# Performance work log

Hardware: AMD Instinct MI355X
Metric: run time of the kernel (lower is better)

The kernel has to match this reference:

```python
import jax, jax.numpy as jnp
import numpy as np

HID, H, D, DFF = 128, 4, 128, 2048   # hidden_dim, nheads, out_feats per head, dim_feedforward
N, E, B = 32768, 524288, 32
EPS = 1e-5
SLOPE = 0.2  # DGL EdgeGATConv negative_slope default


def setup_inputs() -> dict:
    key = jax.random.key(0)
    ks = jax.random.split(key, 16)
    s = 0.05
    return {
        "h": jax.random.normal(ks[0], (N, HID), jnp.float32),
        "e": jax.random.normal(ks[1], (E, 1), jnp.float32),
        "src": jax.random.randint(ks[2], (E,), 0, N, jnp.int32),
        "dst": jax.random.randint(ks[3], (E,), 0, N, jnp.int32),
        "batch_size": B,
        # EdgeGATConv params (fc / fc_edge / res_fc are bias-free in DGL)
        "W_fc": jax.random.normal(ks[4], (HID, H * D), jnp.float32) * s,
        "attn_l": jax.random.normal(ks[5], (H, D), jnp.float32) * s,
        "attn_r": jax.random.normal(ks[6], (H, D), jnp.float32) * s,
        "W_fe": jax.random.normal(ks[7], (1, H * D), jnp.float32) * s,
        "attn_e": jax.random.normal(ks[8], (H, D), jnp.float32) * s,
        "W_res": jax.random.normal(ks[9], (HID, H * D), jnp.float32) * s,
        "gat_bias": jnp.zeros((H * D,), jnp.float32),
        # linear_mha + norms + FFN
        "W_mha": jax.random.normal(ks[10], (H * D, HID), jnp.float32) * s,
        "b_mha": jnp.zeros((HID,), jnp.float32),
        "n1_g": jnp.ones((HID,), jnp.float32),
        "n1_b": jnp.zeros((HID,), jnp.float32),
        "n2_g": jnp.ones((HID,), jnp.float32),
        "n2_b": jnp.zeros((HID,), jnp.float32),
        "W1": jax.random.normal(ks[11], (HID, DFF), jnp.float32) * s,
        "b1": jnp.zeros((DFF,), jnp.float32),
        "W2": jax.random.normal(ks[12], (DFF, HID), jnp.float32) * s,
        "b2": jnp.zeros((HID,), jnp.float32),
    }


def _ln(x, g, b):
    mu = x.mean(-1, keepdims=True)
    var = ((x - mu) ** 2).mean(-1, keepdims=True)
    return (x - mu) * jax.lax.rsqrt(var + EPS) * g + b


def reference(h, e, src, dst, batch_size, W_fc, attn_l, attn_r, W_fe, attn_e,
              W_res, gat_bias, W_mha, b_mha, n1_g, n1_b, n2_g, n2_b,
              W1, b1, W2, b2):
    n = h.shape[0]
    h0 = h
    # --- EdgeGATConv (eval mode: dropouts are identity) ---
    ft = (h @ W_fc).reshape(n, H, D)                         # (N,H,D)
    el = jnp.einsum("nhd,hd->nh", ft, attn_l)                # (N,H)
    er = jnp.einsum("nhd,hd->nh", ft, attn_r)
    fe = (e @ W_fe).reshape(-1, H, D)                        # (E,H,D)
    ee = jnp.einsum("ehd,hd->eh", fe, attn_e)                # (E,H)
    sc = jax.nn.leaky_relu(el[src] + er[dst] + ee, SLOPE)    # (E,H)
    # segment softmax over incoming edges of each dst node
    m = jax.ops.segment_max(sc, dst, num_segments=n)         # (N,H)
    m = jnp.where(jnp.isfinite(m), m, 0.0)                   # empty segments
    w = jnp.exp(sc - m[dst])
    z = jax.ops.segment_sum(w, dst, num_segments=n)
    zd = z[dst]
    alpha = w / jnp.where(zd == 0, 1.0, zd)                  # (E,H)
    msg = ft[src] * alpha[:, :, None]                        # (E,H,D)
    rst = jax.ops.segment_sum(msg, dst, num_segments=n)      # (N,H,D)
    rst = rst + (h0 @ W_res).reshape(n, H, D) + gat_bias.reshape(1, H, D)
    # --- transformer wrapper ---
    x = jax.nn.relu(rst).reshape(n, H * D)
    x = jax.nn.relu(x @ W_mha + b_mha)
    x = _ln(h0 + x, n1_g, n1_b)
    x = x.reshape(batch_size, -1, x.shape[1])                # (B, N/B, HID)
    ff = jax.nn.relu(x @ W1 + b1) @ W2 + b2
    return _ln(x + ff, n2_g, n2_b)
```

## Files before the change

kernel.cpp:

```cpp
#include <hip/hip_runtime.h>
#include <hip/hip_bf16.h>

#define N_NODES 32768
#define E_EDGES 524288
#define HIDDIM 128
#define FDIM 512
#define DFF 2048
#define LN_EPS 1e-5f
#define SLOPE 0.2f
#define CAP 64

typedef __bf16 bf16_t;
typedef __bf16 bf16x8 __attribute__((ext_vector_type(8)));
typedef float f32x4 __attribute__((ext_vector_type(4)));
typedef float f32x2 __attribute__((ext_vector_type(2)));

#define GLD_LDS16(gp, lp) __builtin_amdgcn_global_load_lds( \
    (const __attribute__((address_space(1))) unsigned int*)(gp), \
    (__attribute__((address_space(3))) unsigned int*)(lp), 16, 0, 0)

__device__ inline unsigned char f32_to_e4m3(float v) {
#if __has_builtin(__builtin_amdgcn_cvt_pk_fp8_f32)
    return (unsigned char)(__builtin_amdgcn_cvt_pk_fp8_f32(v, v, 0, false) & 0xff);
#else
    unsigned bits = __float_as_uint(v);
    unsigned sign = (bits >> 24) & 0x80;
    float av = fabsf(v);
    if (av >= 448.f) return (unsigned char)(sign | 0x7E);
    int e = (int)((bits >> 23) & 0xFF) - 127;
    if (e < -6) { int n = (int)rintf(av * 512.f); return (unsigned char)(sign | n); }
    float ulp = exp2f((float)(e - 3));
    int n = (int)rintf(av / ulp);
    if (n == 16) { e += 1; n = 8; }
    return (unsigned char)(sign | ((e + 7) << 3) | (n - 8));
#endif
}
template<bool HI>
__device__ inline f32x2 e4m3x2_to_f32(unsigned u) {
#if __has_builtin(__builtin_amdgcn_cvt_pk_f32_fp8)
    return __builtin_amdgcn_cvt_pk_f32_fp8(u, HI);
#else
    f32x2 r;
    unsigned b0 = HI ? ((u >> 16) & 0xff) : (u & 0xff);
    unsigned b1 = HI ? ((u >> 24) & 0xff) : ((u >> 8) & 0xff);
    unsigned bs[2] = {b0, b1};
    for (int i = 0; i < 2; ++i) {
        unsigned b = bs[i];
        float s = (b & 0x80) ? -1.f : 1.f;
        int e = (b >> 3) & 15, m = b & 7;
        float v = e ? (8 + m) * exp2f((float)(e - 10)) : m * exp2f(-9.f);
        r[i] = s * v;
    }
    return r;
#endif
}

__device__ inline void pack_range(const float* __restrict__ B, bf16_t* __restrict__ out,
                                  int id, int N) {
    const int g = id / N, n = id % N;
    union { bf16_t b[8]; uint4 u; } pk;
#pragma unroll
    for (int j = 0; j < 8; ++j) pk.b[j] = (bf16_t)B[(size_t)(g * 8 + j) * N + n];
    *(uint4*)(out + (size_t)id * 8) = pk.u;
}

__global__ __launch_bounds__(256) void prep_kernel(const float* __restrict__ h, bf16_t* __restrict__ hb,
                                                   const float* __restrict__ W_fc, bf16_t* __restrict__ Wfc_p,
                                                   const float* __restrict__ W_res, bf16_t* __restrict__ Wres_p,
                                                   const float* __restrict__ W_mha, bf16_t* __restrict__ Wmha_p,
                                                   const float* __restrict__ W1, bf16_t* __restrict__ W1_p,
                                                   const float* __restrict__ W2, bf16_t* __restrict__ W2_p,
                                                   const float* __restrict__ W_fe, const float* __restrict__ attn_e,
                                                   float* __restrict__ ce) {
    int bid = blockIdx.x;
    const int tid = threadIdx.x;
    if (bid < 4096) {
        const int id = bid * 256 + tid;
        const float4 v = ((const float4*)h)[id];
        union { bf16_t b[4]; uint2 u; } pk;
        pk.b[0] = (bf16_t)v.x; pk.b[1] = (bf16_t)v.y; pk.b[2] = (bf16_t)v.z; pk.b[3] = (bf16_t)v.w;
        *(uint2*)(hb + (size_t)id * 4) = pk.u;
        return;
    }
    bid -= 4096;
    if (bid < 32)  { pack_range(W_fc,  Wfc_p,  bid * 256 + tid, 512);  return; }
    bid -= 32;
    if (bid < 32)  { pack_range(W_res, Wres_p, bid * 256 + tid, 512);  return; }
    bid -= 32;
    if (bid < 32)  { pack_range(W_mha, Wmha_p, bid * 256 + tid, 128);  return; }
    bid -= 32;
    if (bid < 128) { pack_range(W1,    W1_p,   bid * 256 + tid, 2048); return; }
    bid -= 128;
    if (bid < 128) { pack_range(W2,    W2_p,   bid * 256 + tid, 128);  return; }
    if (tid < 128) {
        const float4 w = ((const float4*)W_fe)[tid];
        const float4 a = ((const float4*)attn_e)[tid];
        float p = w.x * a.x + w.y * a.y + w.z * a.z + w.w * a.w;
        for (int off = 16; off; off >>= 1) p += __shfl_down(p, off, 32);
        if ((tid & 31) == 0) ce[tid >> 5] = p;
    }
}

__global__ __launch_bounds__(256, 2) void gemm_ftres(const bf16_t* __restrict__ A,
                                                     const bf16_t* __restrict__ Bf,
                                                     const bf16_t* __restrict__ Brs,
                                                     const float* __restrict__ attn_l,
                                                     const float* __restrict__ attn_r,
                                                     unsigned char* __restrict__ ft8,
                                                     float* __restrict__ el,
                                                     float* __restrict__ er,
                                                     bf16_t* __restrict__ res) {
    __shared__ __align__(16) bf16_t lA[4096];
    __shared__ __align__(16) bf16_t lBf[4096];
    __shared__ __align__(16) bf16_t lBr[4096];
    __shared__ float s_el[2][128], s_er[2][128];
    const int tid = threadIdx.x, lane = tid & 63, wave = tid >> 6;
    const int wm = (wave >> 1) * 64, wn = (wave & 1) * 64;
    const int row0 = blockIdx.y * 128;
    const int head = blockIdx.x, col0 = head * 128;
    const int ko = lane >> 4, rl = lane & 15;
    f32x4 accf[4][4] = {};
    f32x4 accr[4][4] = {};
    const int c0 = tid, c1 = tid + 256;
    const int g0 = c0 >> 7, m0 = c0 & 127;
    const int g1 = c1 >> 7, m1 = c1 & 127;
    for (int k0 = 0; k0 < 128; k0 += 32) {
        __syncthreads();
        GLD_LDS16(A + (size_t)(row0 + m0) * 128 + k0 + g0 * 8, lA + c0 * 8);
        GLD_LDS16(A + (size_t)(row0 + m1) * 128 + k0 + g1 * 8, lA + c1 * 8);
        GLD_LDS16(Bf + ((size_t)(k0 / 8 + g0) * 512 + col0 + m0) * 8, lBf + c0 * 8);
        GLD_LDS16(Bf + ((size_t)(k0 / 8 + g1) * 512 + col0 + m1) * 8, lBf + c1 * 8);
        GLD_LDS16(Brs + ((size_t)(k0 / 8 + g0) * 512 + col0 + m0) * 8, lBr + c0 * 8);
        GLD_LDS16(Brs + ((size_t)(k0 / 8 + g1) * 512 + col0 + m1) * 8, lBr + c1 * 8);
        __syncthreads();
        bf16x8 af[4], bff[4], bfr[4];
#pragma unroll
        for (int i = 0; i < 4; ++i) {
            af[i]  = *(const bf16x8*)&lA[(ko * 128 + wm + i * 16 + rl) * 8];
            bff[i] = *(const bf16x8*)&lBf[(ko * 128 + wn + i * 16 + rl) * 8];
            bfr[i] = *(const bf16x8*)&lBr[(ko * 128 + wn + i * 16 + rl) * 8];
        }
#pragma unroll
        for (int i = 0; i < 4; ++i)
#pragma unroll
            for (int j = 0; j < 4; ++j) {
                accf[i][j] = __builtin_amdgcn_mfma_f32_16x16x32_bf16(af[i], bff[j], accf[i][j], 0, 0, 0);
                accr[i][j] = __builtin_amdgcn_mfma_f32_16x16x32_bf16(af[i], bfr[j], accr[i][j], 0, 0, 0);
            }
    }
    const int cr = (lane >> 4) * 4, cc = lane & 15;
    float al[4], ar[4];
#pragma unroll
    for (int j = 0; j < 4; ++j) {
        al[j] = attn_l[col0 + wn + j * 16 + cc];
        ar[j] = attn_r[col0 + wn + j * 16 + cc];
    }
#pragma unroll
    for (int i = 0; i < 4; ++i)
#pragma unroll
        for (int r = 0; r < 4; ++r) {
            const int row = row0 + wm + i * 16 + cr + r;
            float pel = 0.f, per = 0.f;
#pragma unroll
            for (int j = 0; j < 4; ++j) {
                const int col = col0 + wn + j * 16 + cc;
                const float v = accf[i][j][r];
                ft8[(size_t)row * 512 + col] = f32_to_e4m3(v);
                res[(size_t)row * 512 + col] = (bf16_t)accr[i][j][r];
                pel += v * al[j];
                per += v * ar[j];
            }
#pragma unroll
            for (int m = 1; m < 16; m <<= 1) {
                pel += __shfl_xor(pel, m);
                per += __shfl_xor(per, m);
            }
            if (cc == 0) {
                s_el[wn >> 6][wm + i * 16 + cr + r] = pel;
                s_er[wn >> 6][wm + i * 16 + cr + r] = per;
            }
        }
    __syncthreads();
    if (tid < 128) {
        el[(size_t)(row0 + tid) * 4 + head] = s_el[0][tid] + s_el[1][tid];
        er[(size_t)(row0 + tid) * 4 + head] = s_er[0][tid] + s_er[1][tid];
    }
}

__global__ __launch_bounds__(256) void gemm_mha_ln(const bf16_t* __restrict__ A,
                                                   const bf16_t* __restrict__ Bp,
                                                   const float* __restrict__ bias,
                                                   const float* __restrict__ h0,
                                                   const float* __restrict__ gamma,
                                                   const float* __restrict__ beta,
                                                   bf16_t* __restrict__ out) {
    __shared__ __align__(16) bf16_t lA[4096];
    __shared__ __align__(16) bf16_t lB[4096];
    __shared__ float s_s1[2][128], s_s2[2][128], s_mu[128], s_rs[128];
    const int tid = threadIdx.x, lane = tid & 63, wave = tid >> 6;
    const int wm = (wave >> 1) * 64, wn = (wave & 1) * 64;
    const int row0 = blockIdx.x * 128;
    const int ko = lane >> 4, rl = lane & 15;
    f32x4 acc[4][4] = {};
    const int c0 = tid, c1 = tid + 256;
    const int g0 = c0 >> 7, m0 = c0 & 127;
    const int g1 = c1 >> 7, m1 = c1 & 127;
    for (int k0 = 0; k0 < 512; k0 += 32) {
        __syncthreads();
        GLD_LDS16(A + (size_t)(row0 + m0) * 512 + k0 + g0 * 8, lA + c0 * 8);
        GLD_LDS16(A + (size_t)(row0 + m1) * 512 + k0 + g1 * 8, lA + c1 * 8);
        GLD_LDS16(Bp + ((size_t)(k0 / 8 + g0) * 128 + m0) * 8, lB + c0 * 8);
        GLD_LDS16(Bp + ((size_t)(k0 / 8 + g1) * 128 + m1) * 8, lB + c1 * 8);
        __syncthreads();
        bf16x8 af[4], bfr[4];
#pragma unroll
        for (int i = 0; i < 4; ++i) {
            af[i]  = *(const bf16x8*)&lA[(ko * 128 + wm + i * 16 + rl) * 8];
            bfr[i] = *(const bf16x8*)&lB[(ko * 128 + wn + i * 16 + rl) * 8];
        }
#pragma unroll
        for (int i = 0; i < 4; ++i)
#pragma unroll
            for (int j = 0; j < 4; ++j)
                acc[i][j] = __builtin_amdgcn_mfma_f32_16x16x32_bf16(af[i], bfr[j], acc[i][j], 0, 0, 0);
    }
    const int cr = (lane >> 4) * 4, cc = lane & 15;
#pragma unroll
    for (int j = 0; j < 4; ++j) {
        const int col = wn + j * 16 + cc;
        const float bb = bias[col];
#pragma unroll
        for (int i = 0; i < 4; ++i)
#pragma unroll
            for (int r = 0; r < 4; ++r) {
                const int row = row0 + wm + i * 16 + cr + r;
                acc[i][j][r] = fmaxf(acc[i][j][r] + bb, 0.f) + h0[(size_t)row * 128 + col];
            }
    }
#pragma unroll
    for (int i = 0; i < 4; ++i)
#pragma unroll
        for (int r = 0; r < 4; ++r) {
            float s1 = 0.f, s2 = 0.f;
#pragma unroll
            for (int j = 0; j < 4; ++j) { const float v = acc[i][j][r]; s1 += v; s2 += v * v; }
#pragma unroll
            for (int m = 1; m < 16; m <<= 1) {
                s1 += __shfl_xor(s1, m);
                s2 += __shfl_xor(s2, m);
            }
            if (cc == 0) {
                s_s1[wn >> 6][wm + i * 16 + cr + r] = s1;
                s_s2[wn >> 6][wm + i * 16 + cr + r] = s2;
            }
        }
    __syncthreads();
    if (tid < 128) {
        const float a = s_s1[0][tid] + s_s1[1][tid];
        const float q = s_s2[0][tid] + s_s2[1][tid];
        const float mu = a * (1.f / 128.f);
        s_mu[tid] = mu;
        s_rs[tid] = rsqrtf(q * (1.f / 128.f) - mu * mu + LN_EPS);
    }
    __syncthreads();
#pragma unroll
    for (int j = 0; j < 4; ++j) {
        const int col = wn + j * 16 + cc;
        const float gg = gamma[col], bb = beta[col];
#pragma unroll
        for (int i = 0; i < 4; ++i)
#pragma unroll
            for (int r = 0; r < 4; ++r) {
                const int rloc = wm + i * 16 + cr + r;
                out[(size_t)(row0 + rloc) * 128 + col] =
                    (bf16_t)((acc[i][j][r] - s_mu[rloc]) * s_rs[rloc] * gg + bb);
            }
    }
}

__global__ __launch_bounds__(512, 2) void ffn_fused(const bf16_t* __restrict__ x3,
                                                    const bf16_t* __restrict__ W1p,
                                                    const float* __restrict__ b1,
                                                    const bf16_t* __restrict__ W2p,
                                                    const float* __restrict__ b2,
                                                    const float* __restrict__ gamma,
                                                    const float* __restrict__ beta,
                                                    float* __restrict__ out) {
    __shared__ __align__(16) bf16_t lW1[3][8192];
    __shared__ __align__(16) bf16_t lW2[4][8192];
    __shared__ __align__(16) bf16_t lY[2][8192];
    __shared__ float s_s1[2][128], s_s2[2][128], s_mu[128], s_rs[128];
    const int tid = threadIdx.x, lane = tid & 63, wave = tid >> 6;
    const int wr  = (wave >> 1) * 32;
    const int wc1 = (wave & 1) * 32;
    const int wc2 = (wave & 1) * 64;
    const int row0 = blockIdx.x * 128;
    const int ko = lane >> 4, rl = lane & 15;
    const int cr = ko * 4, cc = rl;

    bf16_t* lX = &lW1[0][0];
#pragma unroll
    for (int it = 0; it < 4; ++it) {
        const int c = it * 512 + tid, g = c >> 7, m = c & 127;
        GLD_LDS16(x3 + (size_t)(row0 + m) * 128 + g * 8, lX + c * 8);
    }
    __syncthreads();
    bf16x8 afx[2][4];
#pragma unroll
    for (int i = 0; i < 2; ++i)
#pragma unroll
        for (int kk = 0; kk < 4; ++kk)
            afx[i][kk] = *(const bf16x8*)&lX[((kk * 4 + ko) * 128 + wr + i * 16 + rl) * 8];
    asm volatile("s_waitcnt lgkmcnt(0)" ::: "memory");
    __builtin_amdgcn_s_barrier();
    __builtin_amdgcn_sched_barrier(0);

    auto stage_chunk = [&](int chn, bf16_t* w1d, bf16_t* w2d) {
#pragma unroll
        for (int it = 0; it < 2; ++it) {
            const int c = it * 512 + tid, g = c >> 6, n = c & 63;
            GLD_LDS16(W1p + ((size_t)g * 2048 + chn * 64 + n) * 8, w1d + c * 8);
        }
#pragma unroll
        for (int it = 0; it < 2; ++it) {
            const int c = it * 512 + tid, g = c >> 7, n = c & 127;
            GLD_LDS16(W2p + ((size_t)(chn * 8 + g) * 128 + n) * 8, w2d + c * 8);
        }
    };

    f32x4 xacc[2][4] = {};

    auto gemm1 = [&](int chn, const bf16_t* w1c, bf16_t* ydst) {
        f32x4 yacc[2][2] = {};
        __builtin_amdgcn_s_setprio(1);
#pragma unroll
        for (int kk = 0; kk < 4; ++kk) {
            bf16x8 bw[2];
#pragma unroll
            for (int jd = 0; jd < 2; ++jd)
                bw[jd] = *(const bf16x8*)&w1c[((kk * 4 + ko) * 64 + wc1 + jd * 16 + rl) * 8];
#pragma unroll
            for (int jd = 0; jd < 2; ++jd)
#pragma unroll
                for (int ir = 0; ir < 2; ++ir)
                    yacc[jd][ir] = __builtin_amdgcn_mfma_f32_16x16x32_bf16(bw[jd], afx[ir][kk], yacc[jd][ir], 0, 0, 0);
        }
        __builtin_amdgcn_s_setprio(0);
#pragma unroll
        for (int jd = 0; jd < 2; ++jd) {
            const int dffb = wc1 + jd * 16 + cr;
            const float4 bb = *(const float4*)(b1 + chn * 64 + dffb);
#pragma unroll
            for (int ir = 0; ir < 2; ++ir) {
                const int rowx = wr + ir * 16 + cc;
                union { bf16_t b[4]; uint2 u; } pk;
                pk.b[0] = (bf16_t)fmaxf(yacc[jd][ir][0] + bb.x, 0.f);
                pk.b[1] = (bf16_t)fmaxf(yacc[jd][ir][1] + bb.y, 0.f);
                pk.b[2] = (bf16_t)fmaxf(yacc[jd][ir][2] + bb.z, 0.f);
                pk.b[3] = (bf16_t)fmaxf(yacc[jd][ir][3] + bb.w, 0.f);
                *(uint2*)&ydst[((dffb >> 3) * 128 + rowx) * 8 + (dffb & 7)] = pk.u;
            }
        }
    };

    auto gemm2 = [&](const bf16_t* w2c, const bf16_t* ysrc) {
        __builtin_amdgcn_s_setprio(1);
#pragma unroll
        for (int kk = 0; kk < 2; ++kk) {
            bf16x8 ay[2], bw2[4];
#pragma unroll
            for (int ir = 0; ir < 2; ++ir)
                ay[ir] = *(const bf16x8*)&ysrc[((kk * 4 + ko) * 128 + wr + ir * 16 + rl) * 8];
#pragma unroll
            for (int j = 0; j < 4; ++j)
                bw2[j] = *(const bf16x8*)&w2c[((kk * 4 + ko) * 128 + wc2 + j * 16 + rl) * 8];
#pragma unroll
            for (int ir = 0; ir < 2; ++ir)
#pragma unroll
                for (int j = 0; j < 4; ++j)
                    xacc[ir][j] = __builtin_amdgcn_mfma_f32_16x16x32_bf16(ay[ir], bw2[j], xacc[ir][j], 0, 0, 0);
        }
        __builtin_amdgcn_s_setprio(0);
    };

#pragma unroll
    for (int pc = 0; pc < 2; ++pc)
        stage_chunk(pc, lW1[pc], lW2[pc]);
    asm volatile("s_waitcnt vmcnt(4)" ::: "memory");
    __builtin_amdgcn_s_barrier();
    __builtin_amdgcn_sched_barrier(0);

    stage_chunk(2, lW1[2], lW2[2]);
    gemm1(0, lW1[0], lY[0]);
    __builtin_amdgcn_sched_barrier(0);
    asm volatile("s_waitcnt vmcnt(4) lgkmcnt(0)" ::: "memory");
    __builtin_amdgcn_s_barrier();
    __builtin_amdgcn_sched_barrier(0);

    int r1 = 1, s1 = 0, r2 = 0, s2 = 3, p = 1;
#pragma unroll 1
    for (int i = 1; i < 32; ++i) {
        if (i < 30)
            stage_chunk(i + 2, lW1[s1], lW2[s2]);
        gemm1(i, lW1[r1], lY[p]);
        gemm2(lW2[r2], lY[p ^ 1]);
        __builtin_amdgcn_sched_barrier(0);
        if (i < 30)
            asm volatile("s_waitcnt vmcnt(4) lgkmcnt(0)" ::: "memory");
        else if (i == 30)
            asm volatile("s_waitcnt vmcnt(2) lgkmcnt(0)" ::: "memory");
        else
            asm volatile("s_waitcnt vmcnt(0) lgkmcnt(0)" ::: "memory");
        __builtin_amdgcn_s_barrier();
        __builtin_amdgcn_sched_barrier(0);
        r1 = (r1 == 2) ? 0 : r1 + 1;
        s1 = (s1 == 2) ? 0 : s1 + 1;
        r2 = (r2 == 3) ? 0 : r2 + 1;
        s2 = (s2 == 3) ? 0 : s2 + 1;
        p ^= 1;
    }
    gemm2(lW2[3], lY[1]);

#pragma unroll
    for (int j = 0; j < 4; ++j) {
        const int col = wc2 + j * 16 + cc;
        const float bb = b2[col];
#pragma unroll
        for (int ir = 0; ir < 2; ++ir)
#pragma unroll
            for (int r = 0; r < 4; ++r) {
                const int row = wr + ir * 16 + cr + r;
                xacc[ir][j][r] += bb + (float)x3[(size_t)(row0 + row) * 128 + col];
            }
    }
#pragma unroll
    for (int ir = 0; ir < 2; ++ir)
#pragma unroll
        for (int r = 0; r < 4; ++r) {
            float s1v = 0.f, s2v = 0.f;
#pragma unroll
            for (int j = 0; j < 4; ++j) { const float v = xacc[ir][j][r]; s1v += v; s2v += v * v; }
#pragma unroll
            for (int m = 1; m < 16; m <<= 1) {
                s1v += __shfl_xor(s1v, m);
                s2v += __shfl_xor(s2v, m);
            }
            if (cc == 0) {
                s_s1[wave & 1][wr + ir * 16 + cr + r] = s1v;
                s_s2[wave & 1][wr + ir * 16 + cr + r] = s2v;
            }
        }
    __syncthreads();
    if (tid < 128) {
        const float a = s_s1[0][tid] + s_s1[1][tid];
        const float q = s_s2[0][tid] + s_s2[1][tid];
        const float mu = a * (1.f / 128.f);
        s_mu[tid] = mu;
        s_rs[tid] = rsqrtf(q * (1.f / 128.f) - mu * mu + LN_EPS);
    }
    __syncthreads();
#pragma unroll
    for (int j = 0; j < 4; ++j) {
        const int col = wc2 + j * 16 + cc;
        const float gg = gamma[col], bb = beta[col];
#pragma unroll
        for (int ir = 0; ir < 2; ++ir)
#pragma unroll
            for (int r = 0; r < 4; ++r) {
                const int rloc = wr + ir * 16 + cr + r;
                out[(size_t)(row0 + rloc) * 128 + col] =
                    (xacc[ir][j][r] - s_mu[rloc]) * s_rs[rloc] * gg + bb;
            }
    }
}

__global__ __launch_bounds__(256) void edge_build(const float* __restrict__ evals,
                                                  const int* __restrict__ src,
                                                  const int* __restrict__ dst,
                                                  const float* __restrict__ el,
                                                  const float* __restrict__ er,
                                                  const float* __restrict__ ce,
                                                  int* __restrict__ cursor,
                                                  int* __restrict__ csr_src,
                                                  float4* __restrict__ csr_w) {
    const int e = blockIdx.x * 256 + threadIdx.x;
    const int s = src[e], d = dst[e];
    const float ev = evals[e];
    const float4 l = *(const float4*)(el + (size_t)s * 4);
    const float4 r = *(const float4*)(er + (size_t)d * 4);
    const float4 c = *(const float4*)ce;
    float4 w;
    {
        float v;
        v = l.x + r.x + ev * c.x; v = v >= 0.f ? v : SLOPE * v; w.x = __expf(v);
        v = l.y + r.y + ev * c.y; v = v >= 0.f ? v : SLOPE * v; w.y = __expf(v);
        v = l.z + r.z + ev * c.z; v = v >= 0.f ? v : SLOPE * v; w.z = __expf(v);
        v = l.w + r.w + ev * c.w; v = v >= 0.f ? v : SLOPE * v; w.w = __expf(v);
    }
    const int pos = atomicAdd(&cursor[d], 1);
    if (pos < CAP) {
        csr_src[(size_t)d * CAP + pos] = s;
        csr_w[(size_t)d * CAP + pos] = w;
    }
}

__global__ __launch_bounds__(128) void aggregate_kernel(const unsigned char* __restrict__ ft8,
                                                        const bf16_t* __restrict__ res,
                                                        const int* __restrict__ cursor,
                                                        const int* __restrict__ csr_src,
                                                        const float4* __restrict__ csr_w,
                                                        const float* __restrict__ gat_bias,
                                                        bf16_t* __restrict__ x1) {
    const int n = blockIdx.x, t = threadIdx.x;
    __shared__ int s_src[CAP];
    __shared__ float s_w[CAP][4];
    const int deg = min(cursor[n], CAP);
    const int ht = t >> 5;
    if (t < deg) {
        s_src[t] = csr_src[(size_t)n * CAP + t];
        *(float4*)s_w[t] = csr_w[(size_t)n * CAP + t];
    }
    __syncthreads();
    float4 acc = {0.f, 0.f, 0.f, 0.f};
    float z = 0.f;
    for (int j = 0; j < deg; ++j) {
        const float w = s_w[j][ht];
        z += w;
        const unsigned u = *(const unsigned*)(ft8 + (size_t)s_src[j] * 512 + t * 4);
        const f32x2 lo = e4m3x2_to_f32<false>(u);
        const f32x2 hi = e4m3x2_to_f32<true>(u);
        acc.x += w * lo[0]; acc.y += w * lo[1];
        acc.z += w * hi[0]; acc.w += w * hi[1];
    }
    const float rz = deg > 0 ? 1.f / z : 0.f;
    const uint2 ur = *(const uint2*)(res + (size_t)n * FDIM + t * 4);
    const float4 gb = ((const float4*)gat_bias)[t];
    union { bf16_t b[4]; uint2 u; } pk;
    pk.b[0] = (bf16_t)fmaxf(acc.x * rz + __uint_as_float(ur.x << 16) + gb.x, 0.f);
    pk.b[1] = (bf16_t)fmaxf(acc.y * rz + __uint_as_float(ur.x & 0xFFFF0000u) + gb.y, 0.f);
    pk.b[2] = (bf16_t)fmaxf(acc.z * rz + __uint_as_float(ur.y << 16) + gb.z, 0.f);
    pk.b[3] = (bf16_t)fmaxf(acc.w * rz + __uint_as_float(ur.y & 0xFFFF0000u) + gb.w, 0.f);
    *(uint2*)(x1 + (size_t)n * FDIM + t * 4) = pk.u;
}

extern "C" void kernel_launch(void* const* d_in, const int* in_sizes, int n_in,
                              void* d_out, int out_size, void* d_ws, size_t ws_size,
                              hipStream_t stream) {
    const float* h        = (const float*)d_in[0];
    const float* evals    = (const float*)d_in[1];
    const int*   src      = (const int*)d_in[2];
    const int*   dst      = (const int*)d_in[3];
    const float* W_fc     = (const float*)d_in[5];
    const float* attn_l   = (const float*)d_in[6];
    const float* attn_r   = (const float*)d_in[7];
    const float* W_fe     = (const float*)d_in[8];
    const float* attn_e   = (const float*)d_in[9];
    const float* W_res    = (const float*)d_in[10];
    const float* gat_bias = (const float*)d_in[11];
    const float* W_mha    = (const float*)d_in[12];
    const float* b_mha    = (const float*)d_in[13];
    const float* n1_g     = (const float*)d_in[14];
    const float* n1_b     = (const float*)d_in[15];
    const float* n2_g     = (const float*)d_in[16];
    const float* n2_b     = (const float*)d_in[17];
    const float* W1       = (const float*)d_in[18];
    const float* b1       = (const float*)d_in[19];
    const float* W2       = (const float*)d_in[20];
    const float* b2       = (const float*)d_in[21];

    char* ws = (char*)d_ws;
    unsigned char* ft8 = (unsigned char*)(ws + 0);
    bf16_t* res     = (bf16_t*)(ws + 16777216ull);
    bf16_t* x1      = (bf16_t*)(ws + 50331648ull);
    float4* csr_w   = (float4*)(ws + 83886080ull);
    int*    csr_src = (int*)   (ws + 117440512ull);
    bf16_t* x3b     = (bf16_t*)(ws + 125829120ull);
    bf16_t* hb      = (bf16_t*)(ws + 134217728ull);
    bf16_t* Wfc_p   = (bf16_t*)(ws + 142606336ull);
    bf16_t* Wres_p  = (bf16_t*)(ws + 142737408ull);
    bf16_t* Wmha_p  = (bf16_t*)(ws + 142868480ull);
    bf16_t* W1_p    = (bf16_t*)(ws + 142999552ull);
    bf16_t* W2_p    = (bf16_t*)(ws + 143523840ull);
    float*  el      = (float*) (ws + 144048128ull);
    float*  er      = (float*) (ws + 144572416ull);
    float*  ce      = (float*) (ws + 145096704ull);
    int*    cursor  = (int*)   (ws + 145096768ull);

    if (ws_size < 146000000ull) return;

    (void)hipMemsetAsync(cursor, 0, 131072, stream);

    prep_kernel<<<4449, 256, 0, stream>>>(h, hb, W_fc, Wfc_p, W_res, Wres_p,
                                          W_mha, Wmha_p, W1, W1_p, W2, W2_p,
                                          W_fe, attn_e, ce);
    gemm_ftres<<<dim3(4, 256), 256, 0, stream>>>(hb, Wfc_p, Wres_p, attn_l, attn_r, ft8, el, er, res);
    edge_build<<<E_EDGES / 256, 256, 0, stream>>>(evals, src, dst, el, er, ce, cursor, csr_src, csr_w);
    aggregate_kernel<<<N_NODES, 128, 0, stream>>>(ft8, res, cursor, csr_src, csr_w, gat_bias, x1);
    gemm_mha_ln<<<256, 256, 0, stream>>>(x1, Wmha_p, b_mha, h, n1_g, n1_b, x3b);
    ffn_fused<<<256, 512, 0, stream>>>(x3b, W1_p, b1, W2_p, b2, n2_g, n2_b, (float*)d_out);
}
```

Before: 291.1 us.

## Re-tile FFN waves to 64-row tiles with split-K gemm2 and LDS reduction

The fused FFN kernel now gives each wave a 64-row tile. In gemm1 each wave owns a 16-column slice of the DFF chunk. In gemm2 each wave computes a 64x64 output tile over half of the K chunk, so every loaded LDS fragment feeds more MFMAs. The two K-halves of the gemm2 accumulator are summed through LDS scratch at the end, and only half the waves then do the LayerNorm epilogue. This raises accumulator register pressure (64 f32 per lane for xacc plus 16 A fragments) against 2 blocks per SM, and adds a final reduction step.

```diff
diff --git a/kernel.cpp b/kernel.cpp
--- a/kernel.cpp
+++ b/kernel.cpp
@@ -291,9 +291,13 @@
     __shared__ __align__(16) bf16_t lY[2][8192];
     __shared__ float s_s1[2][128], s_s2[2][128], s_mu[128], s_rs[128];
     const int tid = threadIdx.x, lane = tid & 63, wave = tid >> 6;
-    const int wr  = (wave >> 1) * 32;
-    const int wc1 = (wave & 1) * 32;
-    const int wc2 = (wave & 1) * 64;
+    const int kh  = wave & 1;
+    const int ds  = wave & 3;
+    const int cg  = (wave >> 1) & 1;
+    const int rg  = wave >> 2;
+    const int wr  = rg * 64;
+    const int wc1 = ds * 16;
+    const int wc2 = cg * 64;
     const int row0 = blockIdx.x * 128;
     const int ko = lane >> 4, rl = lane & 15;
     const int cr = ko * 4, cc = rl;
@@ -305,12 +309,12 @@
         GLD_LDS16(x3 + (size_t)(row0 + m) * 128 + g * 8, lX + c * 8);
     }
     __syncthreads();
-    bf16x8 afx[2][4];
-#pragma unroll
-    for (int i = 0; i < 2; ++i)
+    bf16x8 afx[4][4];
+#pragma unroll
+    for (int ir = 0; ir < 4; ++ir)
 #pragma unroll
         for (int kk = 0; kk < 4; ++kk)
-            afx[i][kk] = *(const bf16x8*)&lX[((kk * 4 + ko) * 128 + wr + i * 16 + rl) * 8];
+            afx[ir][kk] = *(const bf16x8*)&lX[((kk * 4 + ko) * 128 + wr + ir * 16 + rl) * 8];
     asm volatile("s_waitcnt lgkmcnt(0)" ::: "memory");
     __builtin_amdgcn_s_barrier();
     __builtin_amdgcn_sched_barrier(0);
@@ -328,58 +332,47 @@
         }
     };
 
-    f32x4 xacc[2][4] = {};
+    f32x4 xacc[4][4] = {};
 
     auto gemm1 = [&](int chn, const bf16_t* w1c, bf16_t* ydst) {
-        f32x4 yacc[2][2] = {};
+        f32x4 yacc[4] = {};
         __builtin_amdgcn_s_setprio(1);
 #pragma unroll
         for (int kk = 0; kk < 4; ++kk) {
-            bf16x8 bw[2];
-#pragma unroll
-            for (int jd = 0; jd < 2; ++jd)
-                bw[jd] = *(const bf16x8*)&w1c[((kk * 4 + ko) * 64 + wc1 + jd * 16 + rl) * 8];
-#pragma unroll
-            for (int jd = 0; jd < 2; ++jd)
-#pragma unroll
-                for (int ir = 0; ir < 2; ++ir)
-                    yacc[jd][ir] = __builtin_amdgcn_mfma_f32_16x16x32_bf16(bw[jd], afx[ir][kk], yacc[jd][ir], 0, 0, 0);
+            const bf16x8 bw = *(const bf16x8*)&w1c[((kk * 4 + ko) * 64 + wc1 + rl) * 8];
+#pragma unroll
+            for (int ir = 0; ir < 4; ++ir)
+                yacc[ir] = __builtin_amdgcn_mfma_f32_16x16x32_bf16(bw, afx[ir][kk], yacc[ir], 0, 0, 0);
         }
         __builtin_amdgcn_s_setprio(0);
-#pragma unroll
-        for (int jd = 0; jd < 2; ++jd) {
-            const int dffb = wc1 + jd * 16 + cr;
-            const float4 bb = *(const float4*)(b1 + chn * 64 + dffb);
-#pragma unroll
-            for (int ir = 0; ir < 2; ++ir) {
-                const int rowx = wr + ir * 16 + cc;
-                union { bf16_t b[4]; uint2 u; } pk;
-                pk.b[0] = (bf16_t)fmaxf(yacc[jd][ir][0] + bb.x, 0.f);
-                pk.b[1] = (bf16_t)fmaxf(yacc[jd][ir][1] + bb.y, 0.f);
-                pk.b[2] = (bf16_t)fmaxf(yacc[jd][ir][2] + bb.z, 0.f);
-                pk.b[3] = (bf16_t)fmaxf(yacc[jd][ir][3] + bb.w, 0.f);
-                *(uint2*)&ydst[((dffb >> 3) * 128 + rowx) * 8 + (dffb & 7)] = pk.u;
-            }
+        const int dffb = wc1 + cr;
+        const float4 bb = *(const float4*)(b1 + chn * 64 + dffb);
+#pragma unroll
+        for (int ir = 0; ir < 4; ++ir) {
+            const int rowx = wr + ir * 16 + cc;
+            union { bf16_t b[4]; uint2 u; } pk;
+            pk.b[0] = (bf16_t)fmaxf(yacc[ir][0] + bb.x, 0.f);
+            pk.b[1] = (bf16_t)fmaxf(yacc[ir][1] + bb.y, 0.f);
+            pk.b[2] = (bf16_t)fmaxf(yacc[ir][2] + bb.z, 0.f);
+            pk.b[3] = (bf16_t)fmaxf(yacc[ir][3] + bb.w, 0.f);
+            *(uint2*)&ydst[((dffb >> 3) * 128 + rowx) * 8 + (dffb & 7)] = pk.u;
         }
     };
 
     auto gemm2 = [&](const bf16_t* w2c, const bf16_t* ysrc) {
+        bf16x8 ay[4], bw2[4];
+#pragma unroll
+        for (int ir = 0; ir < 4; ++ir)
+            ay[ir] = *(const bf16x8*)&ysrc[((kh * 4 + ko) * 128 + wr + ir * 16 + rl) * 8];
+#pragma unroll
+        for (int j = 0; j < 4; ++j)
+            bw2[j] = *(const bf16x8*)&w2c[((kh * 4 + ko) * 128 + wc2 + j * 16 + rl) * 8];
         __builtin_amdgcn_s_setprio(1);
 #pragma unroll
-        for (int kk = 0; kk < 2; ++kk) {
-            bf16x8 ay[2], bw2[4];
-#pragma unroll
-            for (int ir = 0; ir < 2; ++ir)
-                ay[ir] = *(const bf16x8*)&ysrc[((kk * 4 + ko) * 128 + wr + ir * 16 + rl) * 8];
+        for (int ir = 0; ir < 4; ++ir)
 #pragma unroll
             for (int j = 0; j < 4; ++j)
-                bw2[j] = *(const bf16x8*)&w2c[((kk * 4 + ko) * 128 + wc2 + j * 16 + rl) * 8];
-#pragma unroll
-            for (int ir = 0; ir < 2; ++ir)
-#pragma unroll
-                for (int j = 0; j < 4; ++j)
-                    xacc[ir][j] = __builtin_amdgcn_mfma_f32_16x16x32_bf16(ay[ir], bw2[j], xacc[ir][j], 0, 0, 0);
-        }
+                xacc[ir][j] = __builtin_amdgcn_mfma_f32_16x16x32_bf16(ay[ir], bw2[j], xacc[ir][j], 0, 0, 0);
         __builtin_amdgcn_s_setprio(0);
     };
 
@@ -397,11 +390,11 @@
     __builtin_amdgcn_s_barrier();
     __builtin_amdgcn_sched_barrier(0);
 
-    int r1 = 1, s1 = 0, r2 = 0, s2 = 3, p = 1;
+    int r1 = 1, sb1 = 0, r2 = 0, sb2 = 3, p = 1;
 #pragma unroll 1
     for (int i = 1; i < 32; ++i) {
         if (i < 30)
-            stage_chunk(i + 2, lW1[s1], lW2[s2]);
+            stage_chunk(i + 2, lW1[sb1], lW2[sb2]);
         gemm1(i, lW1[r1], lY[p]);
         gemm2(lW2[r2], lY[p ^ 1]);
         __builtin_amdgcn_sched_barrier(0);
@@ -414,42 +407,66 @@
         __builtin_amdgcn_s_barrier();
         __builtin_amdgcn_sched_barrier(0);
         r1 = (r1 == 2) ? 0 : r1 + 1;
-        s1 = (s1 == 2) ? 0 : s1 + 1;
+        sb1 = (sb1 == 2) ? 0 : sb1 + 1;
         r2 = (r2 == 3) ? 0 : r2 + 1;
-        s2 = (s2 == 3) ? 0 : s2 + 1;
+        sb2 = (sb2 == 3) ? 0 : sb2 + 1;
         p ^= 1;
     }
     gemm2(lW2[3], lY[1]);
 
-#pragma unroll
-    for (int j = 0; j < 4; ++j) {
-        const int col = wc2 + j * 16 + cc;
-        const float bb = b2[col];
-#pragma unroll
-        for (int ir = 0; ir < 2; ++ir)
+    __syncthreads();
+    {
+        const int q = (wave >> 1) & 3;
+        float* scr = (q < 2) ? ((float*)&lW1[0][0] + q * 4352)
+                             : ((float*)&lW2[0][0] + (q - 2) * 4352);
+        if (kh) {
+#pragma unroll
+            for (int ir = 0; ir < 4; ++ir)
+#pragma unroll
+                for (int j = 0; j < 4; ++j)
+                    *(f32x4*)(scr + lane * 68 + (ir * 4 + j) * 4) = xacc[ir][j];
+        }
+        __syncthreads();
+        if (!kh) {
+#pragma unroll
+            for (int ir = 0; ir < 4; ++ir)
+#pragma unroll
+                for (int j = 0; j < 4; ++j)
+                    xacc[ir][j] += *(const f32x4*)(scr + lane * 68 + (ir * 4 + j) * 4);
+        }
+    }
+
+    if (!kh) {
+#pragma unroll
+        for (int j = 0; j < 4; ++j) {
+            const int col = wc2 + j * 16 + cc;
+            const float bb = b2[col];
+#pragma unroll
+            for (int ir = 0; ir < 4; ++ir)
+#pragma unroll
+                for (int r = 0; r < 4; ++r) {
+                    const int row = wr + ir * 16 + cr + r;
+                    xacc[ir][j][r] += bb + (float)x3[(size_t)(row0 + row) * 128 + col];
+                }
+        }
+#pragma unroll
+        for (int ir = 0; ir < 4; ++ir)
 #pragma unroll
             for (int r = 0; r < 4; ++r) {
-                const int row = wr + ir * 16 + cr + r;
-                xacc[ir][j][r] += bb + (float)x3[(size_t)(row0 + row) * 128 + col];
-            }
-    }
-#pragma unroll
-    for (int ir = 0; ir < 2; ++ir)
-#pragma unroll
-        for (int r = 0; r < 4; ++r) {
-            float s1v = 0.f, s2v = 0.f;
-#pragma unroll
-            for (int j = 0; j < 4; ++j) { const float v = xacc[ir][j][r]; s1v += v; s2v += v * v; }
-#pragma unroll
-            for (int m = 1; m < 16; m <<= 1) {
-                s1v += __shfl_xor(s1v, m);
-                s2v += __shfl_xor(s2v, m);
-            }
-            if (cc == 0) {
-                s_s1[wave & 1][wr + ir * 16 + cr + r] = s1v;
-                s_s2[wave & 1][wr + ir * 16 + cr + r] = s2v;
-            }
-        }
+                float s1v = 0.f, s2v = 0.f;
+#pragma unroll
+                for (int j = 0; j < 4; ++j) { const float v = xacc[ir][j][r]; s1v += v; s2v += v * v; }
+#pragma unroll
+                for (int m = 1; m < 16; m <<= 1) {
+                    s1v += __shfl_xor(s1v, m);
+                    s2v += __shfl_xor(s2v, m);
+                }
+                if (cc == 0) {
+                    s_s1[cg][wr + ir * 16 + cr + r] = s1v;
+                    s_s2[cg][wr + ir * 16 + cr + r] = s2v;
+                }
+            }
+    }
     __syncthreads();
     if (tid < 128) {
         const float a = s_s1[0][tid] + s_s1[1][tid];
@@ -459,18 +476,20 @@
         s_rs[tid] = rsqrtf(q * (1.f / 128.f) - mu * mu + LN_EPS);
     }
     __syncthreads();
-#pragma unroll
-    for (int j = 0; j < 4; ++j) {
-        const int col = wc2 + j * 16 + cc;
-        const float gg = gamma[col], bb = beta[col];
-#pragma unroll
-        for (int ir = 0; ir < 2; ++ir)
-#pragma unroll
-            for (int r = 0; r < 4; ++r) {
-                const int rloc = wr + ir * 16 + cr + r;
-                out[(size_t)(row0 + rloc) * 128 + col] =
-                    (xacc[ir][j][r] - s_mu[rloc]) * s_rs[rloc] * gg + bb;
-            }
+    if (!kh) {
+#pragma unroll
+        for (int j = 0; j < 4; ++j) {
+            const int col = wc2 + j * 16 + cc;
+            const float gg = gamma[col], bb = beta[col];
+#pragma unroll
+            for (int ir = 0; ir < 4; ++ir)
+#pragma unroll
+                for (int r = 0; r < 4; ++r) {
+                    const int rloc = wr + ir * 16 + cr + r;
+                    out[(size_t)(row0 + rloc) * 128 + col] =
+                        (xacc[ir][j][r] - s_mu[rloc]) * s_rs[rloc] * gg + bb;
+                }
+        }
     }
 }
 
```

Result: no change. 288.0 us (-1.1%).
